# Kernel tuning notes

Measured on AMD Instinct MI355X. Metric: run time of the kernel, lower is better.

The kernel has to match this reference:

```python
import jax, jax.numpy as jnp
import numpy as np

KAPPA = 1.0
SIGMA = 0.3
EPS = 1e-5  # torch BatchNorm1d default eps


def _bn(y, g, b):
    # training-mode batch norm: biased batch statistics over the batch axis
    mu = jnp.mean(y, axis=0)
    var = jnp.mean((y - mu) ** 2, axis=0)
    return g * (y - mu) * jax.lax.rsqrt(var + EPS) + b


def _hid(x, W, b, g, be):
    # Linear -> BatchNorm1d -> ReLU
    return jax.nn.relu(_bn(x @ W + b, g, be))


def setup_inputs() -> dict:
    key = jax.random.key(0)
    ks = jax.random.split(key, 12)
    B, D, H, T = 2048, 256, 266, 51  # H = dim + 10
    S = T - 1
    sc = jnp.float32(0.1)
    f32 = jnp.float32
    inp = {}
    inp["x"] = jax.random.normal(ks[0], (B, D), f32)
    inp["dW"] = jax.random.normal(ks[1], (S, B, D), f32)   # hoisted per-step noise xi
    inp["law"] = jax.random.normal(ks[2], (S, D), f32)
    inp["timegrid"] = jnp.linspace(0.0, 1.0, T).astype(f32)
    # per-timestep MLP stacks (i_h1 / h1_h2 / h2_o)
    inp["W1"] = sc * jax.random.normal(ks[3], (S, D, H), f32)
    inp["b1"] = jnp.zeros((S, H), f32)
    inp["g1"] = jnp.ones((S, H), f32)
    inp["be1"] = jnp.zeros((S, H), f32)
    inp["W2"] = sc * jax.random.normal(ks[4], (S, H, H), f32)
    inp["b2"] = jnp.zeros((S, H), f32)
    inp["g2"] = jnp.ones((S, H), f32)
    inp["be2"] = jnp.zeros((S, H), f32)
    inp["W3"] = sc * jax.random.normal(ks[5], (S, H, D), f32)
    inp["b3"] = jnp.zeros((S, D), f32)
    # v0 network (v0_i_h1 / v0_h1_h2 / v0_h2_o, all Linear+BN+ReLU)
    inp["Wv1"] = sc * jax.random.normal(ks[6], (D, H), f32)
    inp["bv1"] = jnp.zeros((H,), f32)
    inp["gv1"] = jnp.ones((H,), f32)
    inp["bev1"] = jnp.zeros((H,), f32)
    inp["Wv2"] = sc * jax.random.normal(ks[7], (H, H), f32)
    inp["bv2"] = jnp.zeros((H,), f32)
    inp["gv2"] = jnp.ones((H,), f32)
    inp["bev2"] = jnp.zeros((H,), f32)
    inp["Wv3"] = sc * jax.random.normal(ks[8], (H, 1), f32)
    inp["bv3"] = jnp.zeros((1,), f32)
    inp["gv3"] = jnp.ones((1,), f32)
    inp["bev3"] = jnp.zeros((1,), f32)
    return inp


def reference(x, dW, law, timegrid,
              W1, b1, g1, be1, W2, b2, g2, be2, W3, b3,
              Wv1, bv1, gv1, bev1, Wv2, bv2, gv2, bev2, Wv3, bv3, gv3, bev3):
    hgrid = jnp.diff(timegrid)  # [S]
    # v0 network evaluated on the initial state (note: last stage is also Linear+BN+ReLU)
    v0 = _hid(_hid(_hid(x, Wv1, bv1, gv1, bev1), Wv2, bv2, gv2, bev2), Wv3, bv3, gv3, bev3)  # [B,1]

    def step(carry, xs):
        xc, v = carry
        w1, bb1, gg1, bbe1, w2, bb2, gg2, bbe2, w3, bb3, li, dw, h = xs
        h1 = _hid(xc, w1, bb1, gg1, bbe1)
        h2 = _hid(h1, w2, bb2, gg2, bbe2)
        grad = h2 @ w3 + bb3                                   # [B,D]
        # f = kappa^2/2 * ||x - law_i||^2 + 1/2 * ||alpha||^2,  alpha = -grad
        f = 0.5 * KAPPA ** 2 * jnp.sum((xc - li) ** 2, axis=1) + 0.5 * jnp.sum(grad ** 2, axis=1)
        noise = SIGMA * jnp.sqrt(h) * dw                       # [B,D]
        # diag(grad @ noise^T) == rowwise dot product: O(B*D) instead of O(B^2*D)
        v = v - (f * h)[:, None] + jnp.sum(grad * noise, axis=1, keepdims=True)
        xc = xc - grad * h + noise
        return (xc, v), None

    (x_final, v), _ = jax.lax.scan(
        step, (x, v0),
        (W1, b1, g1, be1, W2, b2, g2, be2, W3, b3, law, dW, hgrid))
    return v  # [B,1]; (x_final and the path are byproducts of the same scan)
```

## Files before the change

### kernel.cpp

```cpp
#include <hip/hip_runtime.h>
#include <hip/hip_bf16.h>


#define BATCH 2048
#define DD    256
#define HH    266
#define HP    272
#define SS    50
#define BN_EPS 1e-5f
#define SIG   0.3f
#define AS_STRIDE 296

#define XC_OFF 0
#define Y1_OFF 524288
#define Y2_OFF 1081344
#define V_OFF  1638400
#define S1_OFF 1640448
#define S2_OFF 1649152
#define S1V_OFF 1657856
#define S2V_OFF 1662208
#define SV_OFF  1666560
#define WQ_OFF  1666576

#define W1S 69632
#define W2S 78336
#define W3S 73728
#define W1Q_OFF 0
#define W2Q_OFF 3481600
#define W3Q_OFF 7398400
#define WV1Q_OFF 11084800
#define WV2Q_OFF 11154432

#define BAR_OFF 7283200

typedef unsigned short ushort_t;
using short8 = __attribute__((ext_vector_type(8))) short;
using f32x4  = __attribute__((ext_vector_type(4))) float;

__device__ __forceinline__ ushort_t f2b(float f) {
    unsigned u = __float_as_uint(f);
    unsigned r = u + 0x7FFF + ((u >> 16) & 1);
    return (ushort_t)(r >> 16);
}

__device__ __forceinline__ float ld_coh(const float* p) {
    return __hip_atomic_load((const float*)p, __ATOMIC_RELAXED, __HIP_MEMORY_SCOPE_AGENT);
}

__device__ __forceinline__ void prefetch16(const void* p, int n16, int tid) {
    const f32x4* q = (const f32x4*)p;
    for (int i = tid; i < n16; i += 512) {
        f32x4 t = q[i];
        asm volatile("" :: "v"(t));
    }
}

__global__ __launch_bounds__(256) void k_conv(const float* __restrict__ src,
                                              ushort_t* __restrict__ dst,
                                              int K, int N, int KT, int NT,
                                              long total) {
    long t = (long)blockIdx.x * 256 + threadIdx.x;
    if (t >= total) return;
    int per = KT * NT * 512;
    int step = (int)(t / per);
    int e = (int)(t - (long)step * per);
    int kt = e / (NT * 512);
    int r = e - kt * NT * 512;
    int nt = r / 512;
    int r2 = r & 511;
    int lane = r2 >> 3;
    int j = r2 & 7;
    int k = kt * 32 + (lane >> 4) * 8 + j;
    int n = nt * 16 + (lane & 15);
    float v = (k < K && n < N) ? src[(size_t)step * K * N + (size_t)k * N + n] : 0.f;
    dst[t] = f2b(v);
}

__global__ __launch_bounds__(256) void k_pre(float* __restrict__ ws) {
    unsigned* bar = (unsigned*)(ws + BAR_OFF);
    for (int i = threadIdx.x; i < 512; i += 256) atomicExch(bar + i, 0u);
}

__device__ __forceinline__ void grid_bar(unsigned* bar, unsigned gen, int bid) {
    __syncthreads();
    if (threadIdx.x == 0) {
        unsigned* leaf = bar + (bid & 7) * 32;
        unsigned* root = bar + 256;
        unsigned* rel  = bar + 288;
        bool done = false;
        unsigned a = __hip_atomic_fetch_add(leaf, 1u, __ATOMIC_RELAXED, __HIP_MEMORY_SCOPE_AGENT);
        if (a == gen * 16u + 15u) {
            unsigned r = __hip_atomic_fetch_add(root, 1u, __ATOMIC_RELAXED, __HIP_MEMORY_SCOPE_AGENT);
            if (r == gen * 8u + 7u) {
                __hip_atomic_store(rel, gen + 1u, __ATOMIC_RELAXED, __HIP_MEMORY_SCOPE_AGENT);
                done = true;
            }
        }
        if (!done) {
            while (__hip_atomic_load(rel, __ATOMIC_RELAXED, __HIP_MEMORY_SCOPE_AGENT) < gen + 1u)
                __builtin_amdgcn_s_sleep(1);
        }
        asm volatile("" ::: "memory");
    }
    __syncthreads();
}

__device__ __forceinline__ void compute_ac_coh(const float* __restrict__ si,
                                               const float* __restrict__ g,
                                               const float* __restrict__ be,
                                               float (*AC)[HP]) {
    int t = threadIdx.x;
    if (t < HP) {
        float a = 0.f, c = 0.f;
        if (t < HH) {
            float s = 0.f, q = 0.f;
            #pragma unroll
            for (int r = 0; r < 8; ++r) {
                s += ld_coh(si + r * 544 + t);
                q += ld_coh(si + r * 544 + 272 + t);
            }
            float mu  = s * (1.0f / 2048.0f);
            float var = q * (1.0f / 2048.0f) - mu * mu;
            float rs  = rsqrtf(fmaxf(var, 0.0f) + BN_EPS);
            a = g[t] * rs;
            c = be[t] - mu * a;
        }
        AC[0][t] = a;
        AC[1][t] = c;
    }
}

__device__ __forceinline__ void dev_lin16(
    int bid, int mode, int KT,
    const float* __restrict__ gsrc,
    const float* __restrict__ lsrc,
    const float* __restrict__ stats_in, const float* __restrict__ g,
    const float* __restrict__ be,
    const ushort_t* __restrict__ Wq, const float* __restrict__ bias,
    float* __restrict__ ylds,
    float* __restrict__ stats_out,
    float* __restrict__ zero_ptr,
    ushort_t* __restrict__ As, float (*AC)[HP])
{
    const int tid  = threadIdx.x;
    const int lane = tid & 63;
    const int wv   = tid >> 6;
    const int quad = lane >> 4;
    const int l15  = lane & 15;
    const int row0 = bid * 16;

    if (zero_ptr != nullptr) {
        int z = bid * 512 + tid;
        if (z < 4352) atomicExch(zero_ptr + z, 0.0f);
    }

    if (mode == 2) { compute_ac_coh(stats_in, g, be, AC); __syncthreads(); }

    const int PAIRS = KT * 16;
    for (int idx = tid; idx < 16 * PAIRS; idx += 512) {
        int m  = idx / PAIRS;
        int kk = (idx - m * PAIRS) * 2;
        float v0, v1;
        if (mode == 2) {
            v0 = (kk < HH)   ? fmaxf(fmaf(AC[0][kk],   lsrc[m * HP + kk],   AC[1][kk]),   0.f) : 0.f;
            v1 = (kk+1 < HH) ? fmaxf(fmaf(AC[0][kk+1], lsrc[m * HP + kk+1], AC[1][kk+1]), 0.f) : 0.f;
        } else {
            v0 = gsrc[(size_t)(row0 + m) * DD + kk];
            v1 = gsrc[(size_t)(row0 + m) * DD + kk + 1];
        }
        ((unsigned int*)As)[m * (AS_STRIDE/2) + (kk >> 1)] =
            (unsigned int)f2b(v0) | ((unsigned int)f2b(v1) << 16);
    }
    __syncthreads();

    f32x4 acc[3];
    #pragma unroll
    for (int i = 0; i < 3; ++i) acc[i] = (f32x4){0.f, 0.f, 0.f, 0.f};

    for (int kt = 0; kt < KT; ++kt) {
        short8 af = *(const short8*)(&As[l15 * AS_STRIDE + kt * 32 + quad * 8]);
        const ushort_t* wp = Wq + ((size_t)(kt * 17 + wv)) * 512 + lane * 8;
        #pragma unroll
        for (int i = 0; i < 3; ++i) {
            if (i < 2 || wv == 0) {
                short8 bf = *(const short8*)(wp + (size_t)i * 8 * 512);
                acc[i] = __builtin_amdgcn_mfma_f32_16x16x32_bf16(af, bf, acc[i], 0, 0, 0);
            }
        }
    }

    #pragma unroll
    for (int i = 0; i < 3; ++i) {
        if (i == 2 && wv != 0) continue;
        int t = wv + 8 * i;
        int col = t * 16 + l15;
        float bj = (col < HH) ? bias[col] : 0.f;
        float y0 = acc[i][0] + bj, y1 = acc[i][1] + bj;
        float y2 = acc[i][2] + bj, y3 = acc[i][3] + bj;
        ylds[(quad*4 + 0) * HP + col] = y0;
        ylds[(quad*4 + 1) * HP + col] = y1;
        ylds[(quad*4 + 2) * HP + col] = y2;
        ylds[(quad*4 + 3) * HP + col] = y3;
        float sp = y0 + y1 + y2 + y3;
        float sq = y0*y0 + y1*y1 + y2*y2 + y3*y3;
        sp += __shfl_xor(sp, 16); sp += __shfl_xor(sp, 32);
        sq += __shfl_xor(sq, 16); sq += __shfl_xor(sq, 32);
        if (quad == 0 && col < HH) {
            float* spp = stats_out + (bid & 7) * 544;
            atomicAdd(spp + col, sp);
            atomicAdd(spp + 272 + col, sq);
        }
    }
}

__device__ __forceinline__ void dev_fused16(
    int bid,
    const float* __restrict__ y2l,
    const float* __restrict__ stats_in,
    const float* __restrict__ g2, const float* __restrict__ be2,
    const ushort_t* __restrict__ W3q, const float* __restrict__ b3,
    const float* __restrict__ law, const float* __restrict__ dWs,
    const float* __restrict__ tg, int s, int doP1,
    float* __restrict__ xcl,
    float* __restrict__ vv, float* __restrict__ outv,
    const ushort_t* __restrict__ W1q, const float* __restrict__ b1n,
    float* __restrict__ y1l,
    float* __restrict__ stats_out,
    float* __restrict__ zero_ptr,
    ushort_t* __restrict__ As, float (*AC)[HP], float* __restrict__ red)
{
    const int tid  = threadIdx.x;
    const int lane = tid & 63;
    const int wv   = tid >> 6;
    const int quad = lane >> 4;
    const int l15  = lane & 15;
    const int row0 = bid * 16;

    if (zero_ptr != nullptr) {
        int z = bid * 512 + tid;
        if (z < 4352) atomicExch(zero_ptr + z, 0.0f);
    }

    compute_ac_coh(stats_in, g2, be2, AC);
    __syncthreads();

    for (int idx = tid; idx < 16 * 144; idx += 512) {
        int m  = idx / 144;
        int kk = (idx - m * 144) * 2;
        float v0 = (kk < HH)   ? fmaxf(fmaf(AC[0][kk],   y2l[m * HP + kk],   AC[1][kk]),   0.f) : 0.f;
        float v1 = (kk+1 < HH) ? fmaxf(fmaf(AC[0][kk+1], y2l[m * HP + kk+1], AC[1][kk+1]), 0.f) : 0.f;
        ((unsigned int*)As)[m * (AS_STRIDE/2) + (kk >> 1)] =
            (unsigned int)f2b(v0) | ((unsigned int)f2b(v1) << 16);
    }
    __syncthreads();

    f32x4 acc[2];
    acc[0] = (f32x4){0.f,0.f,0.f,0.f};
    acc[1] = (f32x4){0.f,0.f,0.f,0.f};
    for (int kt = 0; kt < 9; ++kt) {
        short8 af = *(const short8*)(&As[l15 * AS_STRIDE + kt * 32 + quad * 8]);
        const ushort_t* wp = W3q + ((size_t)(kt * 16 + wv)) * 512 + lane * 8;
        acc[0] = __builtin_amdgcn_mfma_f32_16x16x32_bf16(af, *(const short8*)(wp),           acc[0], 0, 0, 0);
        acc[1] = __builtin_amdgcn_mfma_f32_16x16x32_bf16(af, *(const short8*)(wp + 8 * 512), acc[1], 0, 0, 0);
    }

    const float h   = tg[s + 1] - tg[s];
    const float srt = SIG * sqrtf(h);
    float grad[2][4], xcv[2][4], dwv[2][4];
    float sxr[4] = {0,0,0,0}, sgr[4] = {0,0,0,0}, sgnr[4] = {0,0,0,0};
    #pragma unroll
    for (int i = 0; i < 2; ++i) {
        int col = (wv + 8*i) * 16 + l15;
        #pragma unroll
        for (int r = 0; r < 4; ++r) {
            int rl = quad * 4 + r;
            float gd = acc[i][r] + b3[col];
            float xv = xcl[rl * DD + col];
            float dw = dWs[(size_t)(row0 + rl) * DD + col];
            float d  = xv - law[col];
            grad[i][r] = gd; xcv[i][r] = xv; dwv[i][r] = dw;
            sxr[r]  = fmaf(d, d, sxr[r]);
            sgr[r]  = fmaf(gd, gd, sgr[r]);
            sgnr[r] = fmaf(gd, dw, sgnr[r]);
        }
    }
    #pragma unroll
    for (int off = 1; off < 16; off <<= 1) {
        #pragma unroll
        for (int r = 0; r < 4; ++r) {
            sxr[r]  += __shfl_xor(sxr[r],  off);
            sgr[r]  += __shfl_xor(sgr[r],  off);
            sgnr[r] += __shfl_xor(sgnr[r], off);
        }
    }
    if (l15 == 0) {
        #pragma unroll
        for (int r = 0; r < 4; ++r) {
            int rr = quad * 4 + r;
            red[(wv * 16 + rr) * 3 + 0] = sxr[r];
            red[(wv * 16 + rr) * 3 + 1] = sgr[r];
            red[(wv * 16 + rr) * 3 + 2] = sgnr[r];
        }
    }
    __syncthreads();

    if (tid < 16) {
        float sx = 0.f, sg = 0.f, sgn = 0.f;
        #pragma unroll
        for (int w = 0; w < 8; ++w) {
            sx  += red[(w * 16 + tid) * 3 + 0];
            sg  += red[(w * 16 + tid) * 3 + 1];
            sgn += red[(w * 16 + tid) * 3 + 2];
        }
        int row = row0 + tid;
        float f  = 0.5f * (sx + sg);
        float vn = vv[row] - f * h + srt * sgn;
        vv[row] = vn;
        if (s == SS - 1) outv[row] = vn;
    }

    #pragma unroll
    for (int i = 0; i < 2; ++i) {
        int col = (wv + 8*i) * 16 + l15;
        #pragma unroll
        for (int r = 0; r < 4; ++r) {
            int rl = quad * 4 + r;
            float xn = xcv[i][r] - grad[i][r] * h + srt * dwv[i][r];
            xcl[rl * DD + col] = xn;
            if (doP1) As[rl * AS_STRIDE + col] = f2b(xn);
        }
    }
    if (!doP1) return;
    __syncthreads();

    f32x4 acc2[3];
    #pragma unroll
    for (int i = 0; i < 3; ++i) acc2[i] = (f32x4){0.f, 0.f, 0.f, 0.f};
    for (int kt = 0; kt < 8; ++kt) {
        short8 af = *(const short8*)(&As[l15 * AS_STRIDE + kt * 32 + quad * 8]);
        const ushort_t* wp = W1q + ((size_t)(kt * 17 + wv)) * 512 + lane * 8;
        #pragma unroll
        for (int i = 0; i < 3; ++i) {
            if (i < 2 || wv == 0) {
                short8 bf = *(const short8*)(wp + (size_t)i * 8 * 512);
                acc2[i] = __builtin_amdgcn_mfma_f32_16x16x32_bf16(af, bf, acc2[i], 0, 0, 0);
            }
        }
    }
    #pragma unroll
    for (int i = 0; i < 3; ++i) {
        if (i == 2 && wv != 0) continue;
        int t = wv + 8 * i;
        int col = t * 16 + l15;
        float bj = (col < HH) ? b1n[col] : 0.f;
        float y0 = acc2[i][0] + bj, y1 = acc2[i][1] + bj;
        float y2 = acc2[i][2] + bj, y3 = acc2[i][3] + bj;
        y1l[(quad*4 + 0) * HP + col] = y0;
        y1l[(quad*4 + 1) * HP + col] = y1;
        y1l[(quad*4 + 2) * HP + col] = y2;
        y1l[(quad*4 + 3) * HP + col] = y3;
        float sp = y0 + y1 + y2 + y3;
        float sq = y0*y0 + y1*y1 + y2*y2 + y3*y3;
        sp += __shfl_xor(sp, 16); sp += __shfl_xor(sp, 32);
        sq += __shfl_xor(sq, 16); sq += __shfl_xor(sq, 32);
        if (quad == 0 && col < HH) {
            float* spp = stats_out + (bid & 7) * 544;
            atomicAdd(spp + col, sp);
            atomicAdd(spp + 272 + col, sq);
        }
    }
}

__device__ __forceinline__ void dev_v0l3_16(
    int bid, const float* __restrict__ y2l, const float* __restrict__ stats_in,
    const float* __restrict__ gv, const float* __restrict__ bev,
    const float* __restrict__ wv3, const float* __restrict__ bv3,
    float* __restrict__ vout, float* __restrict__ sv,
    float (*AC)[HP], float* __restrict__ xtra)
{
    const int tid = threadIdx.x;
    compute_ac_coh(stats_in, gv, bev, AC);
    __syncthreads();

    const int r   = tid >> 5;
    const int ks  = tid & 31;
    int k0 = ks * 9, k1 = k0 + 9;
    if (k1 > HH) k1 = HH;
    float acc = 0.0f;
    for (int k = k0; k < k1; ++k) {
        float y  = y2l[r * HP + k];
        float a2 = fmaxf(fmaf(AC[0][k], y, AC[1][k]), 0.0f);
        acc = fmaf(a2, wv3[k], acc);
    }
    #pragma unroll
    for (int off = 1; off < 32; off <<= 1) acc += __shfl_xor(acc, off);
    if (ks == 0) {
        float y = acc + bv3[0];
        vout[bid * 16 + r] = y;
        xtra[r] = y;
        xtra[16 + r] = y * y;
    }
    __syncthreads();
    if (tid == 0) {
        float s = 0.f, q = 0.f;
        #pragma unroll
        for (int i = 0; i < 16; ++i) { s += xtra[i]; q += xtra[16 + i]; }
        atomicAdd(sv, s);
        atomicAdd(sv + 1, q);
    }
}

__device__ __forceinline__ void dev_v0fin16(int bid, float* __restrict__ v,
                                            const float* __restrict__ sv,
                                            const float* __restrict__ gv3,
                                            const float* __restrict__ bev3) {
    if (threadIdx.x < 16) {
        float s0 = ld_coh(sv);
        float s1 = ld_coh(sv + 1);
        float mu  = s0 * (1.0f / 2048.0f);
        float var = s1 * (1.0f / 2048.0f) - mu * mu;
        float rs  = rsqrtf(fmaxf(var, 0.0f) + BN_EPS);
        int row = bid * 16 + threadIdx.x;
        float y = v[row];
        v[row] = fmaxf(gv3[0] * (y - mu) * rs + bev3[0], 0.0f);
    }
}

__global__ __launch_bounds__(512) void k_persist(
    const float* __restrict__ x, const float* __restrict__ dW,
    const float* __restrict__ law, const float* __restrict__ tg,
    const float* __restrict__ b1, const float* __restrict__ g1, const float* __restrict__ be1,
    const float* __restrict__ b2, const float* __restrict__ g2, const float* __restrict__ be2,
    const float* __restrict__ b3,
    const float* __restrict__ bv1, const float* __restrict__ gv1, const float* __restrict__ bev1,
    const float* __restrict__ bv2, const float* __restrict__ gv2, const float* __restrict__ bev2,
    const float* __restrict__ Wv3, const float* __restrict__ bv3,
    const float* __restrict__ gv3, const float* __restrict__ bev3,
    float* __restrict__ ws, float* __restrict__ out)
{
    __shared__ ushort_t As[16 * AS_STRIDE];
    __shared__ float AC[2][HP];
    __shared__ float Y1s[16 * HP];
    __shared__ float Y2s[16 * HP];
    __shared__ float XCs[16 * DD];
    __shared__ float XTRA[384];

    const int bid = blockIdx.x;
    const int tid = threadIdx.x;

    float* V   = ws + V_OFF;
    float* S1  = ws + S1_OFF;
    float* S2  = ws + S2_OFF;
    float* S1v = ws + S1V_OFF;
    float* S2v = ws + S2V_OFF;
    float* SV  = ws + SV_OFF;
    ushort_t* WQ = (ushort_t*)(ws + WQ_OFF);
    ushort_t* W1q  = WQ + W1Q_OFF;
    ushort_t* W2q  = WQ + W2Q_OFF;
    ushort_t* W3q  = WQ + W3Q_OFF;
    ushort_t* Wv1q = WQ + WV1Q_OFF;
    ushort_t* Wv2q = WQ + WV2Q_OFF;
    unsigned* bar  = (unsigned*)(ws + BAR_OFF);

    unsigned gen = 0;
    const int sl = (bid >> 3) & 15;

    for (int i = tid; i < 16 * DD; i += 512)
        XCs[i] = x[(size_t)bid * 16 * DD + i];
    {
        int z = bid * 512 + tid;
        if (z < 26128) atomicExch(S1 + z, 0.0f);
    }
    grid_bar(bar, gen, bid); gen++;

    dev_lin16(bid, 0, 8, x, nullptr, nullptr, nullptr, nullptr,
              Wv1q, bv1, Y1s, S1v, nullptr, As, AC);
    grid_bar(bar, gen, bid); gen++;

    dev_lin16(bid, 2, 9, nullptr, Y1s, S1v, gv1, bev1,
              Wv2q, bv2, Y2s, S2v, nullptr, As, AC);
    grid_bar(bar, gen, bid); gen++;

    dev_v0l3_16(bid, Y2s, S2v, gv2, bev2, Wv3, bv3, V, SV, AC, XTRA);
    grid_bar(bar, gen, bid); gen++;

    dev_v0fin16(bid, V, SV, gv3, bev3);
    dev_lin16(bid, 0, 8, x, nullptr, nullptr, nullptr, nullptr,
              W1q, b1, Y1s, S1, nullptr, As, AC);
    prefetch16((const char*)W2q + sl * 9792, 612, tid);
    grid_bar(bar, gen, bid); gen++;

    for (int s = 0; s < SS; ++s) {
        int p = s & 1;
        dev_lin16(bid, 2, 9, nullptr, Y1s, S1 + p * 4352,
                  g1 + s * HH, be1 + s * HH,
                  W2q + (size_t)s * W2S, b2 + s * HH,
                  Y2s, S2 + p * 4352, S1 + (1 - p) * 4352, As, AC);
        prefetch16(dW + (size_t)s * BATCH * DD + (size_t)bid * 16 * DD, 1024, tid);
        prefetch16((const char*)(W3q + (size_t)s * W3S) + sl * 9216, 576, tid);
        if (s + 1 < SS)
            prefetch16((const char*)(W1q + (size_t)(s + 1) * W1S) + sl * 8704, 544, tid);
        grid_bar(bar, gen, bid); gen++;

        int sn = (s + 1 < SS) ? s + 1 : 0;
        dev_fused16(bid, Y2s, S2 + p * 4352,
                    g2 + s * HH, be2 + s * HH,
                    W3q + (size_t)s * W3S, b3 + s * DD,
                    law + s * DD, dW + (size_t)s * BATCH * DD,
                    tg, s, (s < SS - 1) ? 1 : 0,
                    XCs, V, out,
                    W1q + (size_t)sn * W1S, b1 + sn * HH,
                    Y1s, S1 + ((s + 1) & 1) * 4352,
                    S2 + (1 - p) * 4352, As, AC, XTRA);
        if (s + 1 < SS)
            prefetch16((const char*)(W2q + (size_t)(s + 1) * W2S) + sl * 9792, 612, tid);
        grid_bar(bar, gen, bid); gen++;
    }
}

extern "C" void kernel_launch(void* const* d_in, const int* in_sizes, int n_in,
                              void* d_out, int out_size, void* d_ws, size_t ws_size,
                              hipStream_t stream)
{
    (void)in_sizes; (void)n_in; (void)out_size; (void)ws_size;
    const float* x    = (const float*)d_in[0];
    const float* dW   = (const float*)d_in[1];
    const float* law  = (const float*)d_in[2];
    const float* tg   = (const float*)d_in[3];
    const float* W1   = (const float*)d_in[4];
    const float* b1   = (const float*)d_in[5];
    const float* g1   = (const float*)d_in[6];
    const float* be1  = (const float*)d_in[7];
    const float* W2   = (const float*)d_in[8];
    const float* b2   = (const float*)d_in[9];
    const float* g2   = (const float*)d_in[10];
    const float* be2  = (const float*)d_in[11];
    const float* W3   = (const float*)d_in[12];
    const float* b3   = (const float*)d_in[13];
    const float* Wv1  = (const float*)d_in[14];
    const float* bv1  = (const float*)d_in[15];
    const float* gv1  = (const float*)d_in[16];
    const float* bev1 = (const float*)d_in[17];
    const float* Wv2  = (const float*)d_in[18];
    const float* bv2  = (const float*)d_in[19];
    const float* gv2  = (const float*)d_in[20];
    const float* bev2 = (const float*)d_in[21];
    const float* Wv3  = (const float*)d_in[22];
    const float* bv3  = (const float*)d_in[23];
    const float* gv3  = (const float*)d_in[24];
    const float* bev3 = (const float*)d_in[25];

    float* ws = (float*)d_ws;
    ushort_t* WQ = (ushort_t*)(ws + WQ_OFF);
    ushort_t* W1q  = WQ + W1Q_OFF;
    ushort_t* W2q  = WQ + W2Q_OFF;
    ushort_t* W3q  = WQ + W3Q_OFF;
    ushort_t* Wv1q = WQ + WV1Q_OFF;
    ushort_t* Wv2q = WQ + WV2Q_OFF;
    float* out = (float*)d_out;

    k_pre<<<1, 256, 0, stream>>>(ws);
    k_conv<<<13600, 256, 0, stream>>>(W1,  W1q,  DD, HH, 8, 17, (long)SS * W1S);
    k_conv<<<15300, 256, 0, stream>>>(W2,  W2q,  HH, HH, 9, 17, (long)SS * W2S);
    k_conv<<<14400, 256, 0, stream>>>(W3,  W3q,  HH, DD, 9, 16, (long)SS * W3S);
    k_conv<<<272,   256, 0, stream>>>(Wv1, Wv1q, DD, HH, 8, 17, (long)W1S);
    k_conv<<<306,   256, 0, stream>>>(Wv2, Wv2q, HH, HH, 9, 17, (long)W2S);

    k_persist<<<128, 512, 0, stream>>>(
        x, dW, law, tg,
        b1, g1, be1, b2, g2, be2, b3,
        bv1, gv1, bev1, bv2, gv2, bev2,
        Wv3, bv3, gv3, bev3,
        ws, out);
}
```

Measured before the change: 1.319 ms.

## Double persistent block to 1024 threads, one MFMA tile per wave

Raises the persistent kernel from 512 to 1024 threads (16 waves), so each wave computes a single 16-column MFMA tile, with wave 0 also taking the tail tile. The grid barrier gets a separate release flag per leaf to cut spinning contention, and the BN stat reduction uses paired coherent dwordx2 loads. The old L2 prefetch passes are replaced by a single prefetch of dW/law/b3 folded into the first linear stage, and the scratch buffers are reused to free LDS. The risks are register pressure at 1024 threads, and the reduction into Y2s reuses a buffer whose aliasing with later data must stay safe.

```diff
diff --git a/kernel.cpp b/kernel.cpp
--- a/kernel.cpp
+++ b/kernel.cpp
@@ -11,9 +11,6 @@
 #define SIG   0.3f
 #define AS_STRIDE 296
 
-#define XC_OFF 0
-#define Y1_OFF 524288
-#define Y2_OFF 1081344
 #define V_OFF  1638400
 #define S1_OFF 1640448
 #define S2_OFF 1649152
@@ -36,6 +33,7 @@
 typedef unsigned short ushort_t;
 using short8 = __attribute__((ext_vector_type(8))) short;
 using f32x4  = __attribute__((ext_vector_type(4))) float;
+using f32x2  = __attribute__((ext_vector_type(2))) float;
 
 __device__ __forceinline__ ushort_t f2b(float f) {
     unsigned u = __float_as_uint(f);
@@ -46,13 +44,10 @@
 __device__ __forceinline__ float ld_coh(const float* p) {
     return __hip_atomic_load((const float*)p, __ATOMIC_RELAXED, __HIP_MEMORY_SCOPE_AGENT);
 }
-
-__device__ __forceinline__ void prefetch16(const void* p, int n16, int tid) {
-    const f32x4* q = (const f32x4*)p;
-    for (int i = tid; i < n16; i += 512) {
-        f32x4 t = q[i];
-        asm volatile("" :: "v"(t));
-    }
+__device__ __forceinline__ f32x2 ld2_coh(const float* p) {
+    f32x2 v;
+    asm volatile("global_load_dwordx2 %0, %1, off sc0 sc1" : "=v"(v) : "v"(p));
+    return v;
 }
 
 __global__ __launch_bounds__(256) void k_conv(const float* __restrict__ src,
@@ -78,27 +73,30 @@
 
 __global__ __launch_bounds__(256) void k_pre(float* __restrict__ ws) {
     unsigned* bar = (unsigned*)(ws + BAR_OFF);
-    for (int i = threadIdx.x; i < 512; i += 256) atomicExch(bar + i, 0u);
+    for (int i = threadIdx.x; i < 768; i += 256) atomicExch(bar + i, 0u);
 }
 
 __device__ __forceinline__ void grid_bar(unsigned* bar, unsigned gen, int bid) {
     __syncthreads();
     if (threadIdx.x == 0) {
-        unsigned* leaf = bar + (bid & 7) * 32;
+        const int lf = bid & 7;
+        unsigned* leaf = bar + lf * 32;
         unsigned* root = bar + 256;
-        unsigned* rel  = bar + 288;
+        unsigned* rel  = bar + 288 + lf * 32;
         bool done = false;
         unsigned a = __hip_atomic_fetch_add(leaf, 1u, __ATOMIC_RELAXED, __HIP_MEMORY_SCOPE_AGENT);
         if (a == gen * 16u + 15u) {
             unsigned r = __hip_atomic_fetch_add(root, 1u, __ATOMIC_RELAXED, __HIP_MEMORY_SCOPE_AGENT);
             if (r == gen * 8u + 7u) {
-                __hip_atomic_store(rel, gen + 1u, __ATOMIC_RELAXED, __HIP_MEMORY_SCOPE_AGENT);
+                #pragma unroll
+                for (int l = 0; l < 8; ++l)
+                    __hip_atomic_store(bar + 288 + l * 32, gen + 1u, __ATOMIC_RELAXED, __HIP_MEMORY_SCOPE_AGENT);
                 done = true;
             }
         }
         if (!done) {
             while (__hip_atomic_load(rel, __ATOMIC_RELAXED, __HIP_MEMORY_SCOPE_AGENT) < gen + 1u)
-                __builtin_amdgcn_s_sleep(1);
+                __builtin_amdgcn_s_sleep(2);
         }
         asm volatile("" ::: "memory");
     }
@@ -110,36 +108,45 @@
                                                const float* __restrict__ be,
                                                float (*AC)[HP]) {
     int t = threadIdx.x;
-    if (t < HP) {
-        float a = 0.f, c = 0.f;
-        if (t < HH) {
-            float s = 0.f, q = 0.f;
-            #pragma unroll
-            for (int r = 0; r < 8; ++r) {
-                s += ld_coh(si + r * 544 + t);
-                q += ld_coh(si + r * 544 + 272 + t);
+    if (t < 136) {
+        f32x2 sv[8], qv[8];
+        #pragma unroll
+        for (int r = 0; r < 8; ++r) {
+            sv[r] = ld2_coh(si + r * 544 + 2 * t);
+            qv[r] = ld2_coh(si + r * 544 + 272 + 2 * t);
+        }
+        asm volatile("s_waitcnt vmcnt(0)" ::: "memory");
+        __builtin_amdgcn_sched_barrier(0);
+        f32x2 s = sv[0], q = qv[0];
+        #pragma unroll
+        for (int r = 1; r < 8; ++r) { s += sv[r]; q += qv[r]; }
+        #pragma unroll
+        for (int j = 0; j < 2; ++j) {
+            int col = 2 * t + j;
+            float a = 0.f, c = 0.f;
+            if (col < HH) {
+                float mu  = s[j] * (1.0f / 2048.0f);
+                float var = q[j] * (1.0f / 2048.0f) - mu * mu;
+                float rs  = rsqrtf(fmaxf(var, 0.0f) + BN_EPS);
+                a = g[col] * rs;
+                c = be[col] - mu * a;
             }
-            float mu  = s * (1.0f / 2048.0f);
-            float var = q * (1.0f / 2048.0f) - mu * mu;
-            float rs  = rsqrtf(fmaxf(var, 0.0f) + BN_EPS);
-            a = g[t] * rs;
-            c = be[t] - mu * a;
-        }
-        AC[0][t] = a;
-        AC[1][t] = c;
+            AC[0][col] = a;
+            AC[1][col] = c;
+        }
     }
 }
 
 __device__ __forceinline__ void dev_lin16(
     int bid, int mode, int KT,
-    const float* __restrict__ gsrc,
-    const float* __restrict__ lsrc,
+    const float* __restrict__ gsrc, const float* __restrict__ lsrc,
     const float* __restrict__ stats_in, const float* __restrict__ g,
     const float* __restrict__ be,
     const ushort_t* __restrict__ Wq, const float* __restrict__ bias,
-    float* __restrict__ ylds,
-    float* __restrict__ stats_out,
+    float* __restrict__ ylds, float* __restrict__ stats_out,
     float* __restrict__ zero_ptr,
+    const float* __restrict__ pfd, const float* __restrict__ pfl,
+    const float* __restrict__ pfb,
     ushort_t* __restrict__ As, float (*AC)[HP])
 {
     const int tid  = threadIdx.x;
@@ -149,15 +156,22 @@
     const int l15  = lane & 15;
     const int row0 = bid * 16;
 
+    f32x4 pv0 = {0.f,0.f,0.f,0.f}, pv1 = {0.f,0.f,0.f,0.f};
+    if (pfd != nullptr) {
+        pv0 = ((const f32x4*)pfd)[tid];
+        if (tid < 64)        pv1 = ((const f32x4*)pfl)[tid];
+        else if (tid < 128)  pv1 = ((const f32x4*)pfb)[tid - 64];
+    }
+
     if (zero_ptr != nullptr) {
-        int z = bid * 512 + tid;
+        int z = bid * 1024 + tid;
         if (z < 4352) atomicExch(zero_ptr + z, 0.0f);
     }
 
     if (mode == 2) { compute_ac_coh(stats_in, g, be, AC); __syncthreads(); }
 
     const int PAIRS = KT * 16;
-    for (int idx = tid; idx < 16 * PAIRS; idx += 512) {
+    for (int idx = tid; idx < 16 * PAIRS; idx += 1024) {
         int m  = idx / PAIRS;
         int kk = (idx - m * PAIRS) * 2;
         float v0, v1;
@@ -171,32 +185,31 @@
         ((unsigned int*)As)[m * (AS_STRIDE/2) + (kk >> 1)] =
             (unsigned int)f2b(v0) | ((unsigned int)f2b(v1) << 16);
     }
-    __syncthreads();
-
-    f32x4 acc[3];
-    #pragma unroll
-    for (int i = 0; i < 3; ++i) acc[i] = (f32x4){0.f, 0.f, 0.f, 0.f};
-
+    if (pfd != nullptr) {
+        asm volatile("" :: "v"(pv0));
+        if (tid < 128) asm volatile("" :: "v"(pv1));
+    }
+    __syncthreads();
+
+    f32x4 acc0 = {0.f,0.f,0.f,0.f}, acc1 = {0.f,0.f,0.f,0.f};
+    #pragma unroll 3
     for (int kt = 0; kt < KT; ++kt) {
         short8 af = *(const short8*)(&As[l15 * AS_STRIDE + kt * 32 + quad * 8]);
         const ushort_t* wp = Wq + ((size_t)(kt * 17 + wv)) * 512 + lane * 8;
-        #pragma unroll
-        for (int i = 0; i < 3; ++i) {
-            if (i < 2 || wv == 0) {
-                short8 bf = *(const short8*)(wp + (size_t)i * 8 * 512);
-                acc[i] = __builtin_amdgcn_mfma_f32_16x16x32_bf16(af, bf, acc[i], 0, 0, 0);
-            }
+        acc0 = __builtin_amdgcn_mfma_f32_16x16x32_bf16(af, *(const short8*)wp, acc0, 0, 0, 0);
+        if (wv == 0) {
+            const ushort_t* wp2 = Wq + ((size_t)(kt * 17 + 16)) * 512 + lane * 8;
+            acc1 = __builtin_amdgcn_mfma_f32_16x16x32_bf16(af, *(const short8*)wp2, acc1, 0, 0, 0);
         }
     }
 
     #pragma unroll
-    for (int i = 0; i < 3; ++i) {
-        if (i == 2 && wv != 0) continue;
-        int t = wv + 8 * i;
-        int col = t * 16 + l15;
+    for (int i = 0; i < 2; ++i) {
+        if (i == 1 && wv != 0) continue;
+        int col = (i == 0) ? (wv * 16 + l15) : (256 + l15);
+        f32x4 a = (i == 0) ? acc0 : acc1;
         float bj = (col < HH) ? bias[col] : 0.f;
-        float y0 = acc[i][0] + bj, y1 = acc[i][1] + bj;
-        float y2 = acc[i][2] + bj, y3 = acc[i][3] + bj;
+        float y0 = a[0] + bj, y1 = a[1] + bj, y2 = a[2] + bj, y3 = a[3] + bj;
         ylds[(quad*4 + 0) * HP + col] = y0;
         ylds[(quad*4 + 1) * HP + col] = y1;
         ylds[(quad*4 + 2) * HP + col] = y2;
@@ -215,17 +228,14 @@
 
 __device__ __forceinline__ void dev_fused16(
     int bid,
-    const float* __restrict__ y2l,
-    const float* __restrict__ stats_in,
+    const float* __restrict__ y2l, const float* __restrict__ stats_in,
     const float* __restrict__ g2, const float* __restrict__ be2,
     const ushort_t* __restrict__ W3q, const float* __restrict__ b3,
     const float* __restrict__ law, const float* __restrict__ dWs,
     const float* __restrict__ tg, int s, int doP1,
-    float* __restrict__ xcl,
-    float* __restrict__ vv, float* __restrict__ outv,
+    float* __restrict__ xcl, float* __restrict__ vv, float* __restrict__ outv,
     const ushort_t* __restrict__ W1q, const float* __restrict__ b1n,
-    float* __restrict__ y1l,
-    float* __restrict__ stats_out,
+    float* __restrict__ y1l, float* __restrict__ stats_out,
     float* __restrict__ zero_ptr,
     ushort_t* __restrict__ As, float (*AC)[HP], float* __restrict__ red)
 {
@@ -235,16 +245,17 @@
     const int quad = lane >> 4;
     const int l15  = lane & 15;
     const int row0 = bid * 16;
+    const int col  = wv * 16 + l15;
 
     if (zero_ptr != nullptr) {
-        int z = bid * 512 + tid;
+        int z = bid * 1024 + tid;
         if (z < 4352) atomicExch(zero_ptr + z, 0.0f);
     }
 
     compute_ac_coh(stats_in, g2, be2, AC);
     __syncthreads();
 
-    for (int idx = tid; idx < 16 * 144; idx += 512) {
+    for (int idx = tid; idx < 16 * 144; idx += 1024) {
         int m  = idx / 144;
         int kk = (idx - m * 144) * 2;
         float v0 = (kk < HH)   ? fmaxf(fmaf(AC[0][kk],   y2l[m * HP + kk],   AC[1][kk]),   0.f) : 0.f;
@@ -254,35 +265,31 @@
     }
     __syncthreads();
 
-    f32x4 acc[2];
-    acc[0] = (f32x4){0.f,0.f,0.f,0.f};
-    acc[1] = (f32x4){0.f,0.f,0.f,0.f};
+    f32x4 acc = {0.f,0.f,0.f,0.f};
+    #pragma unroll 3
     for (int kt = 0; kt < 9; ++kt) {
         short8 af = *(const short8*)(&As[l15 * AS_STRIDE + kt * 32 + quad * 8]);
         const ushort_t* wp = W3q + ((size_t)(kt * 16 + wv)) * 512 + lane * 8;
-        acc[0] = __builtin_amdgcn_mfma_f32_16x16x32_bf16(af, *(const short8*)(wp),           acc[0], 0, 0, 0);
-        acc[1] = __builtin_amdgcn_mfma_f32_16x16x32_bf16(af, *(const short8*)(wp + 8 * 512), acc[1], 0, 0, 0);
+        acc = __builtin_amdgcn_mfma_f32_16x16x32_bf16(af, *(const short8*)wp, acc, 0, 0, 0);
     }
 
     const float h   = tg[s + 1] - tg[s];
     const float srt = SIG * sqrtf(h);
-    float grad[2][4], xcv[2][4], dwv[2][4];
-    float sxr[4] = {0,0,0,0}, sgr[4] = {0,0,0,0}, sgnr[4] = {0,0,0,0};
+    const float lawv = law[col];
+    const float b3v  = b3[col];
+    float grad[4], xcv[4], dwv[4];
+    float sxr[4], sgr[4], sgnr[4];
     #pragma unroll
-    for (int i = 0; i < 2; ++i) {
-        int col = (wv + 8*i) * 16 + l15;
-        #pragma unroll
-        for (int r = 0; r < 4; ++r) {
-            int rl = quad * 4 + r;
-            float gd = acc[i][r] + b3[col];
-            float xv = xcl[rl * DD + col];
-            float dw = dWs[(size_t)(row0 + rl) * DD + col];
-            float d  = xv - law[col];
-            grad[i][r] = gd; xcv[i][r] = xv; dwv[i][r] = dw;
-            sxr[r]  = fmaf(d, d, sxr[r]);
-            sgr[r]  = fmaf(gd, gd, sgr[r]);
-            sgnr[r] = fmaf(gd, dw, sgnr[r]);
-        }
+    for (int r = 0; r < 4; ++r) {
+        int rl = quad * 4 + r;
+        float gd = acc[r] + b3v;
+        float xv = xcl[rl * DD + col];
+        float dw = dWs[(size_t)(row0 + rl) * DD + col];
+        float d  = xv - lawv;
+        grad[r] = gd; xcv[r] = xv; dwv[r] = dw;
+        sxr[r]  = d * d;
+        sgr[r]  = gd * gd;
+        sgnr[r] = gd * dw;
     }
     #pragma unroll
     for (int off = 1; off < 16; off <<= 1) {
@@ -307,7 +314,7 @@
     if (tid < 16) {
         float sx = 0.f, sg = 0.f, sgn = 0.f;
         #pragma unroll
-        for (int w = 0; w < 8; ++w) {
+        for (int w = 0; w < 16; ++w) {
             sx  += red[(w * 16 + tid) * 3 + 0];
             sg  += red[(w * 16 + tid) * 3 + 1];
             sgn += red[(w * 16 + tid) * 3 + 2];
@@ -320,53 +327,45 @@
     }
 
     #pragma unroll
-    for (int i = 0; i < 2; ++i) {
-        int col = (wv + 8*i) * 16 + l15;
-        #pragma unroll
-        for (int r = 0; r < 4; ++r) {
-            int rl = quad * 4 + r;
-            float xn = xcv[i][r] - grad[i][r] * h + srt * dwv[i][r];
-            xcl[rl * DD + col] = xn;
-            if (doP1) As[rl * AS_STRIDE + col] = f2b(xn);
-        }
+    for (int r = 0; r < 4; ++r) {
+        int rl = quad * 4 + r;
+        float xn = xcv[r] - grad[r] * h + srt * dwv[r];
+        xcl[rl * DD + col] = xn;
+        if (doP1) As[rl * AS_STRIDE + col] = f2b(xn);
     }
     if (!doP1) return;
     __syncthreads();
 
-    f32x4 acc2[3];
-    #pragma unroll
-    for (int i = 0; i < 3; ++i) acc2[i] = (f32x4){0.f, 0.f, 0.f, 0.f};
+    f32x4 a20 = {0.f,0.f,0.f,0.f}, a21 = {0.f,0.f,0.f,0.f};
+    #pragma unroll 4
     for (int kt = 0; kt < 8; ++kt) {
         short8 af = *(const short8*)(&As[l15 * AS_STRIDE + kt * 32 + quad * 8]);
         const ushort_t* wp = W1q + ((size_t)(kt * 17 + wv)) * 512 + lane * 8;
-        #pragma unroll
-        for (int i = 0; i < 3; ++i) {
-            if (i < 2 || wv == 0) {
-                short8 bf = *(const short8*)(wp + (size_t)i * 8 * 512);
-                acc2[i] = __builtin_amdgcn_mfma_f32_16x16x32_bf16(af, bf, acc2[i], 0, 0, 0);
-            }
+        a20 = __builtin_amdgcn_mfma_f32_16x16x32_bf16(af, *(const short8*)wp, a20, 0, 0, 0);
+        if (wv == 0) {
+            const ushort_t* wp2 = W1q + ((size_t)(kt * 17 + 16)) * 512 + lane * 8;
+            a21 = __builtin_amdgcn_mfma_f32_16x16x32_bf16(af, *(const short8*)wp2, a21, 0, 0, 0);
         }
     }
     #pragma unroll
-    for (int i = 0; i < 3; ++i) {
-        if (i == 2 && wv != 0) continue;
-        int t = wv + 8 * i;
-        int col = t * 16 + l15;
-        float bj = (col < HH) ? b1n[col] : 0.f;
-        float y0 = acc2[i][0] + bj, y1 = acc2[i][1] + bj;
-        float y2 = acc2[i][2] + bj, y3 = acc2[i][3] + bj;
-        y1l[(quad*4 + 0) * HP + col] = y0;
-        y1l[(quad*4 + 1) * HP + col] = y1;
-        y1l[(quad*4 + 2) * HP + col] = y2;
-        y1l[(quad*4 + 3) * HP + col] = y3;
+    for (int i = 0; i < 2; ++i) {
+        if (i == 1 && wv != 0) continue;
+        int c2 = (i == 0) ? (wv * 16 + l15) : (256 + l15);
+        f32x4 a = (i == 0) ? a20 : a21;
+        float bj = (c2 < HH) ? b1n[c2] : 0.f;
+        float y0 = a[0] + bj, y1 = a[1] + bj, y2 = a[2] + bj, y3 = a[3] + bj;
+        y1l[(quad*4 + 0) * HP + c2] = y0;
+        y1l[(quad*4 + 1) * HP + c2] = y1;
+        y1l[(quad*4 + 2) * HP + c2] = y2;
+        y1l[(quad*4 + 3) * HP + c2] = y3;
         float sp = y0 + y1 + y2 + y3;
         float sq = y0*y0 + y1*y1 + y2*y2 + y3*y3;
         sp += __shfl_xor(sp, 16); sp += __shfl_xor(sp, 32);
         sq += __shfl_xor(sq, 16); sq += __shfl_xor(sq, 32);
-        if (quad == 0 && col < HH) {
+        if (quad == 0 && c2 < HH) {
             float* spp = stats_out + (bid & 7) * 544;
-            atomicAdd(spp + col, sp);
-            atomicAdd(spp + 272 + col, sq);
+            atomicAdd(spp + c2, sp);
+            atomicAdd(spp + 272 + c2, sq);
         }
     }
 }
@@ -382,23 +381,25 @@
     compute_ac_coh(stats_in, gv, bev, AC);
     __syncthreads();
 
-    const int r   = tid >> 5;
-    const int ks  = tid & 31;
-    int k0 = ks * 9, k1 = k0 + 9;
-    if (k1 > HH) k1 = HH;
-    float acc = 0.0f;
-    for (int k = k0; k < k1; ++k) {
-        float y  = y2l[r * HP + k];
-        float a2 = fmaxf(fmaf(AC[0][k], y, AC[1][k]), 0.0f);
-        acc = fmaf(a2, wv3[k], acc);
-    }
-    #pragma unroll
-    for (int off = 1; off < 32; off <<= 1) acc += __shfl_xor(acc, off);
-    if (ks == 0) {
-        float y = acc + bv3[0];
-        vout[bid * 16 + r] = y;
-        xtra[r] = y;
-        xtra[16 + r] = y * y;
+    if (tid < 512) {
+        const int r  = tid >> 5;
+        const int ks = tid & 31;
+        int k0 = ks * 9, k1 = k0 + 9;
+        if (k1 > HH) k1 = HH;
+        float acc = 0.0f;
+        for (int k = k0; k < k1; ++k) {
+            float y  = y2l[r * HP + k];
+            float a2 = fmaxf(fmaf(AC[0][k], y, AC[1][k]), 0.0f);
+            acc = fmaf(a2, wv3[k], acc);
+        }
+        #pragma unroll
+        for (int off = 1; off < 32; off <<= 1) acc += __shfl_xor(acc, off);
+        if (ks == 0) {
+            float y = acc + bv3[0];
+            vout[bid * 16 + r] = y;
+            xtra[r] = y;
+            xtra[16 + r] = y * y;
+        }
     }
     __syncthreads();
     if (tid == 0) {
@@ -426,7 +427,7 @@
     }
 }
 
-__global__ __launch_bounds__(512) void k_persist(
+__global__ __launch_bounds__(1024) void k_persist(
     const float* __restrict__ x, const float* __restrict__ dW,
     const float* __restrict__ law, const float* __restrict__ tg,
     const float* __restrict__ b1, const float* __restrict__ g1, const float* __restrict__ be1,
@@ -443,7 +444,6 @@
     __shared__ float Y1s[16 * HP];
     __shared__ float Y2s[16 * HP];
     __shared__ float XCs[16 * DD];
-    __shared__ float XTRA[384];
 
     const int bid = blockIdx.x;
     const int tid = threadIdx.x;
@@ -463,31 +463,29 @@
     unsigned* bar  = (unsigned*)(ws + BAR_OFF);
 
     unsigned gen = 0;
-    const int sl = (bid >> 3) & 15;
-
-    for (int i = tid; i < 16 * DD; i += 512)
+
+    for (int i = tid; i < 16 * DD; i += 1024)
         XCs[i] = x[(size_t)bid * 16 * DD + i];
     {
-        int z = bid * 512 + tid;
+        int z = bid * 1024 + tid;
         if (z < 26128) atomicExch(S1 + z, 0.0f);
     }
     grid_bar(bar, gen, bid); gen++;
 
     dev_lin16(bid, 0, 8, x, nullptr, nullptr, nullptr, nullptr,
-              Wv1q, bv1, Y1s, S1v, nullptr, As, AC);
+              Wv1q, bv1, Y1s, S1v, nullptr, nullptr, nullptr, nullptr, As, AC);
     grid_bar(bar, gen, bid); gen++;
 
     dev_lin16(bid, 2, 9, nullptr, Y1s, S1v, gv1, bev1,
-              Wv2q, bv2, Y2s, S2v, nullptr, As, AC);
+              Wv2q, bv2, Y2s, S2v, nullptr, nullptr, nullptr, nullptr, As, AC);
     grid_bar(bar, gen, bid); gen++;
 
-    dev_v0l3_16(bid, Y2s, S2v, gv2, bev2, Wv3, bv3, V, SV, AC, XTRA);
+    dev_v0l3_16(bid, Y2s, S2v, gv2, bev2, Wv3, bv3, V, SV, AC, (float*)As);
     grid_bar(bar, gen, bid); gen++;
 
     dev_v0fin16(bid, V, SV, gv3, bev3);
     dev_lin16(bid, 0, 8, x, nullptr, nullptr, nullptr, nullptr,
-              W1q, b1, Y1s, S1, nullptr, As, AC);
-    prefetch16((const char*)W2q + sl * 9792, 612, tid);
+              W1q, b1, Y1s, S1, nullptr, nullptr, nullptr, nullptr, As, AC);
     grid_bar(bar, gen, bid); gen++;
 
     for (int s = 0; s < SS; ++s) {
@@ -495,11 +493,9 @@
         dev_lin16(bid, 2, 9, nullptr, Y1s, S1 + p * 4352,
                   g1 + s * HH, be1 + s * HH,
                   W2q + (size_t)s * W2S, b2 + s * HH,
-                  Y2s, S2 + p * 4352, S1 + (1 - p) * 4352, As, AC);
-        prefetch16(dW + (size_t)s * BATCH * DD + (size_t)bid * 16 * DD, 1024, tid);
-        prefetch16((const char*)(W3q + (size_t)s * W3S) + sl * 9216, 576, tid);
-        if (s + 1 < SS)
-            prefetch16((const char*)(W1q + (size_t)(s + 1) * W1S) + sl * 8704, 544, tid);
+                  Y2s, S2 + p * 4352, S1 + (1 - p) * 4352,
+                  dW + (size_t)s * BATCH * DD + (size_t)bid * 16 * DD,
+                  law + (size_t)s * DD, b3 + (size_t)s * DD, As, AC);
         grid_bar(bar, gen, bid); gen++;
 
         int sn = (s + 1 < SS) ? s + 1 : 0;
@@ -511,9 +507,7 @@
                     XCs, V, out,
                     W1q + (size_t)sn * W1S, b1 + sn * HH,
                     Y1s, S1 + ((s + 1) & 1) * 4352,
-                    S2 + (1 - p) * 4352, As, AC, XTRA);
-        if (s + 1 < SS)
-            prefetch16((const char*)(W2q + (size_t)(s + 1) * W2S) + sl * 9792, 612, tid);
+                    S2 + (1 - p) * 4352, As, AC, Y2s );
         grid_bar(bar, gen, bid); gen++;
     }
 }
@@ -566,7 +560,7 @@
     k_conv<<<272,   256, 0, stream>>>(Wv1, Wv1q, DD, HH, 8, 17, (long)W1S);
     k_conv<<<306,   256, 0, stream>>>(Wv2, Wv2q, HH, HH, 9, 17, (long)W2S);
 
-    k_persist<<<128, 512, 0, stream>>>(
+    k_persist<<<128, 1024, 0, stream>>>(
         x, dW, law, tg,
         b1, g1, be1, b2, g2, be2, b3,
         bv1, gv1, bev1, bv2, gv2, bev2,
```

New measurement: 1.461 ms. +10.8%, slower.
